# Optimization experiments

Measured on AMD Instinct MI355X. Metric: run time of the kernel, lower is better.

Reference implementation:

```python
import jax, jax.numpy as jnp
import numpy as np


def _layernorm(x, g, b, eps=1e-5):
    mu = jnp.mean(x, axis=-1, keepdims=True)
    var = jnp.mean(jnp.square(x - mu), axis=-1, keepdims=True)
    return (x - mu) * jax.lax.rsqrt(var + eps) * g + b


def setup_inputs() -> dict:
    key = jax.random.key(0)
    ks = jax.random.split(key, 8)
    dim, ctx_dim, heads, dim_head = 256, 256, 8, 64
    inner = heads * dim_head
    s = 0.02
    return {
        "x": jax.random.normal(ks[0], (4, dim, 64, 64), jnp.float32),
        "y": jax.random.normal(ks[1], (4, 1024, ctx_dim), jnp.float32),
        "ln_x_g": jnp.ones((dim,), jnp.float32),
        "ln_x_b": jnp.zeros((dim,), jnp.float32),
        "ln_y_g": jnp.ones((ctx_dim,), jnp.float32),
        "ln_y_b": jnp.zeros((ctx_dim,), jnp.float32),
        "Wq": jax.random.normal(ks[2], (dim, inner), jnp.float32) * s,
        "Wk": jax.random.normal(ks[3], (ctx_dim, inner), jnp.float32) * s,
        "Wv": jax.random.normal(ks[4], (ctx_dim, inner), jnp.float32) * s,
        "bv": jnp.zeros((inner,), jnp.float32),
        "Wo": jax.random.normal(ks[5], (inner, dim), jnp.float32) * s,
        "bo": jnp.zeros((dim,), jnp.float32),
    }


def reference(x, y, ln_x_g, ln_x_b, ln_y_g, ln_y_b, Wq, Wk, Wv, bv, Wo, bo):
    heads, dim_head = 8, 64
    b, c = x.shape[:2]
    # channel_last=False path: [b, c, H, W] -> [b, n, c]
    xn = x.reshape(b, c, -1).swapaxes(1, 2)
    xn = _layernorm(xn, ln_x_g, ln_x_b)          # note: x is reassigned in torch code
    yn = _layernorm(y, ln_y_g, ln_y_b)
    q = xn @ Wq                                   # [b, n, h*d]
    k = yn @ Wk                                   # [b, m, h*d]
    v = yn @ Wv + bv                              # [b, m, h*d]

    def split_heads(t):
        B, N, _ = t.shape
        return t.reshape(B, N, heads, dim_head).transpose(0, 2, 1, 3)  # [b, h, n, d]

    q, k, v = split_heads(q), split_heads(k), split_heads(v)
    attn = jnp.einsum("bhid,bhjd->bhij", q, k) * (dim_head ** -0.5)
    attn = jax.nn.softmax(attn, axis=-1)
    out = jnp.einsum("bhij,bhjd->bhid", attn, v)  # [b, h, n, d]
    out = out.transpose(0, 2, 1, 3).reshape(b, -1, heads * dim_head)
    out = out @ Wo + bo
    return xn + out  # residual with layernormed x (faithful to source)
```

## Files before the change

### kernel.cpp

```cpp
#include <hip/hip_runtime.h>
#include <hip/hip_bf16.h>
#include <cstddef>

#define BATCH 4
#define CDIM 256
#define HW 4096
#define MCTX 1024
#define CTX 256
#define HEADS 8
#define DHEAD 64
#define INNER 512

typedef __attribute__((ext_vector_type(8))) short bf16x8;
typedef __attribute__((ext_vector_type(4))) float f32x4;

static __device__ __forceinline__ ushort f2bf(float f) {
  __hip_bfloat16 h = __float2bfloat16(f);
  return *reinterpret_cast<ushort*>(&h);
}

__global__ __launch_bounds__(256) void ln_x_kernel(
    const float* __restrict__ x, const float* __restrict__ g,
    const float* __restrict__ bta, float* __restrict__ xn,
    ushort* __restrict__ xnbf) {
  const int blk = blockIdx.x;
  const int bi = blk / (HW / 32);
  const int n0 = (blk % (HW / 32)) * 32;
  __shared__ float xt[32][257];
  __shared__ float smu[32], srs[32];
  const int t = threadIdx.x;
  const int nl = t & 31;
  const int c0 = t >> 5;
  const float* xb = x + (size_t)bi * CDIM * HW;
  #pragma unroll
  for (int c = c0; c < CDIM; c += 8)
    xt[nl][c] = xb[(size_t)c * HW + n0 + nl];
  __syncthreads();
  const int col = t >> 3, j = t & 7;
  float s = 0.f, ss = 0.f;
  #pragma unroll
  for (int c = j; c < CDIM; c += 8) {
    float v = xt[col][c];
    s += v; ss += v * v;
  }
  #pragma unroll
  for (int off = 1; off < 8; off <<= 1) {
    s += __shfl_xor(s, off);
    ss += __shfl_xor(ss, off);
  }
  if (j == 0) {
    float mu = s * (1.f / CDIM);
    smu[col] = mu;
    srs[col] = rsqrtf(ss * (1.f / CDIM) - mu * mu + 1e-5f);
  }
  __syncthreads();
  const float gv = g[t], bvv = bta[t];
  float* xnb = xn + ((size_t)bi * HW + n0) * CDIM;
  ushort* xbb = xnbf + ((size_t)bi * HW + n0) * CDIM;
  #pragma unroll 4
  for (int n = 0; n < 32; ++n) {
    float val = (xt[n][t] - smu[n]) * srs[n] * gv + bvv;
    xnb[(size_t)n * CDIM + t] = val;
    xbb[(size_t)n * CDIM + t] = f2bf(val);
  }
}

__global__ __launch_bounds__(256) void ln_y_kernel(
    const float* __restrict__ y, const float* __restrict__ g,
    const float* __restrict__ bta, ushort* __restrict__ ynbf) {
  const int row = blockIdx.x * 4 + (threadIdx.x >> 6);
  const int t = threadIdx.x & 63;
  float4 v = ((const float4*)(y + (size_t)row * CTX))[t];
  float s = v.x + v.y + v.z + v.w;
  float ss = v.x * v.x + v.y * v.y + v.z * v.z + v.w * v.w;
  #pragma unroll
  for (int off = 1; off < 64; off <<= 1) {
    s += __shfl_xor(s, off);
    ss += __shfl_xor(ss, off);
  }
  float mu = s * (1.f / CTX);
  float rs = rsqrtf(ss * (1.f / CTX) - mu * mu + 1e-5f);
  float4 gv = ((const float4*)g)[t];
  float4 b4 = ((const float4*)bta)[t];
  ushort4 ob;
  ob.x = f2bf((v.x - mu) * rs * gv.x + b4.x);
  ob.y = f2bf((v.y - mu) * rs * gv.y + b4.y);
  ob.z = f2bf((v.z - mu) * rs * gv.z + b4.z);
  ob.w = f2bf((v.w - mu) * rs * gv.w + b4.w);
  *(ushort4*)(ynbf + (size_t)row * CTX + t * 4) = ob;
}

static __device__ __forceinline__ void wprep_body(
    const float* __restrict__ W, ushort* __restrict__ Wt, int K, int N) {
  __shared__ ushort T[64][65];
  const int k0 = blockIdx.y * 64, n0 = blockIdx.x * 64;
  const int t = threadIdx.x;
  #pragma unroll
  for (int rr = 0; rr < 4; ++rr) {
    int row = rr * 16 + (t >> 4);
    int c = (t & 15) * 4;
    float4 wv = *(const float4*)(W + (size_t)(k0 + row) * N + n0 + c);
    T[row][c + 0] = f2bf(wv.x); T[row][c + 1] = f2bf(wv.y);
    T[row][c + 2] = f2bf(wv.z); T[row][c + 3] = f2bf(wv.w);
  }
  __syncthreads();
  #pragma unroll
  for (int rr = 0; rr < 4; ++rr) {
    int nrow = rr * 16 + (t >> 4);
    int kc = (t & 15) * 4;
    ushort4 o;
    o.x = T[kc + 0][nrow]; o.y = T[kc + 1][nrow];
    o.z = T[kc + 2][nrow]; o.w = T[kc + 3][nrow];
    *(ushort4*)(Wt + (size_t)(n0 + nrow) * K + k0 + kc) = o;
  }
}

__global__ __launch_bounds__(256) void wprep3_kernel(
    const float* __restrict__ W0, const float* __restrict__ W1,
    const float* __restrict__ W2, ushort* __restrict__ T0,
    ushort* __restrict__ T1, ushort* __restrict__ T2) {
  const int z = blockIdx.z;
  const float* W = (z == 0) ? W0 : (z == 1) ? W1 : W2;
  ushort* Wt = (z == 0) ? T0 : (z == 1) ? T1 : T2;
  wprep_body(W, Wt, 256, 512);
}

__global__ __launch_bounds__(256) void wprep_kernel(
    const float* __restrict__ W, ushort* __restrict__ Wt, int K, int N) {
  wprep_body(W, Wt, K, N);
}

__global__ __launch_bounds__(256) void vtr_kernel(
    const ushort* __restrict__ v, ushort* __restrict__ vt) {
  const int bh = blockIdx.z, bi = bh >> 3, h = bh & 7;
  const int m0 = blockIdx.x * 64;
  __shared__ ushort T[64][65];
  const int t = threadIdx.x;
  #pragma unroll
  for (int rr = 0; rr < 4; ++rr) {
    int row = rr * 16 + (t >> 4);
    int c = (t & 15) * 4;
    ushort4 vv = *(const ushort4*)(v + (size_t)(bi * MCTX + m0 + row) * INNER + h * DHEAD + c);
    T[row][c + 0] = vv.x; T[row][c + 1] = vv.y;
    T[row][c + 2] = vv.z; T[row][c + 3] = vv.w;
  }
  __syncthreads();
  #pragma unroll
  for (int rr = 0; rr < 4; ++rr) {
    int drow = rr * 16 + (t >> 4);
    int mc = (t & 15) * 4;
    ushort4 o;
    o.x = T[mc + 0][drow]; o.y = T[mc + 1][drow];
    o.z = T[mc + 2][drow]; o.w = T[mc + 3][drow];
    *(ushort4*)(vt + (size_t)(bh * 64 + drow) * MCTX + m0 + mc) = o;
  }
}

template <bool HAS_BIAS, bool F32_RES_OUT>
__global__ __launch_bounds__(256) void mfma_gemm(
    const ushort* __restrict__ A, const ushort* __restrict__ Bt,
    const float* __restrict__ bias, const float* __restrict__ res,
    void* __restrict__ Cout, int M, int N, int K, float scale) {
  __shared__ ushort As[128 * 40];
  __shared__ ushort Bs[128 * 40];
  const int t = threadIdx.x;
  const int l = t & 63, w = t >> 6;
  const int lq = l & 15, lg = l >> 4;
  const int wr = w >> 1, wc = w & 1;
  const int m0 = blockIdx.y * 128, n0 = blockIdx.x * 128;
  f32x4 acc[4][4];
  #pragma unroll
  for (int mt = 0; mt < 4; ++mt)
    #pragma unroll
    for (int nt = 0; nt < 4; ++nt)
      #pragma unroll
      for (int e = 0; e < 4; ++e) acc[mt][nt][e] = 0.f;
  const int r = t >> 2, ch = (t & 3) * 8;
  for (int k0 = 0; k0 < K; k0 += 32) {
    uint4 a0 = *(const uint4*)(A + (size_t)(m0 + r) * K + k0 + ch);
    uint4 a1 = *(const uint4*)(A + (size_t)(m0 + r + 64) * K + k0 + ch);
    uint4 b0 = *(const uint4*)(Bt + (size_t)(n0 + r) * K + k0 + ch);
    uint4 b1 = *(const uint4*)(Bt + (size_t)(n0 + r + 64) * K + k0 + ch);
    __syncthreads();
    *(uint4*)(&As[r * 40 + ch]) = a0;
    *(uint4*)(&As[(r + 64) * 40 + ch]) = a1;
    *(uint4*)(&Bs[r * 40 + ch]) = b0;
    *(uint4*)(&Bs[(r + 64) * 40 + ch]) = b1;
    __syncthreads();
    bf16x8 af[4], bfr[4];
    #pragma unroll
    for (int mt = 0; mt < 4; ++mt)
      af[mt] = *(const bf16x8*)(&As[(wr * 64 + mt * 16 + lq) * 40 + lg * 8]);
    #pragma unroll
    for (int nt = 0; nt < 4; ++nt)
      bfr[nt] = *(const bf16x8*)(&Bs[(wc * 64 + nt * 16 + lq) * 40 + lg * 8]);
    #pragma unroll
    for (int mt = 0; mt < 4; ++mt)
      #pragma unroll
      for (int nt = 0; nt < 4; ++nt)
        acc[mt][nt] = __builtin_amdgcn_mfma_f32_16x16x32_bf16(
            af[mt], bfr[nt], acc[mt][nt], 0, 0, 0);
  }
  #pragma unroll
  for (int nt = 0; nt < 4; ++nt) {
    const int colc = n0 + wc * 64 + nt * 16 + lq;
    const float bcol = HAS_BIAS ? bias[colc] : 0.f;
    #pragma unroll
    for (int mt = 0; mt < 4; ++mt) {
      #pragma unroll
      for (int i = 0; i < 4; ++i) {
        const size_t row = (size_t)(m0 + wr * 64 + mt * 16 + lg * 4 + i);
        float v = acc[mt][nt][i] * scale + bcol;
        if (F32_RES_OUT) {
          ((float*)Cout)[row * N + colc] = v + res[row * N + colc];
        } else {
          ((ushort*)Cout)[row * N + colc] = f2bf(v);
        }
      }
    }
  }
}

__global__ __launch_bounds__(512, 4) void attn_mfma(
    const ushort* __restrict__ q, const ushort* __restrict__ k,
    const ushort* __restrict__ vt, ushort* __restrict__ ao) {
  const int bid = blockIdx.x + 16 * (blockIdx.y + 8 * blockIdx.z);
  const int swz = (bid & 7) * 64 + (bid >> 3);
  const int bi = swz >> 7;
  const int h = (swz >> 4) & 7;
  const int n0 = (swz & 15) * 256;
  __shared__ ushort Ks[2][64 * 64];
  __shared__ ushort Vs[2][64 * 64];
  __shared__ ushort Ps[8][2][16 * 64];
  const int t = threadIdx.x;
  const int l = t & 63, w = t >> 6;
  const int lq = l & 15, lg = l >> 4;

  bf16x8 bq[2][2];
  #pragma unroll
  for (int g = 0; g < 2; ++g) {
    const size_t qrow = (size_t)(bi * HW + n0 + w * 32 + g * 16 + lq);
    #pragma unroll
    for (int ks = 0; ks < 2; ++ks)
      bq[g][ks] = *(const bf16x8*)(q + qrow * INNER + h * DHEAD + ks * 32 + lg * 8);
  }

  float m_run[2] = {-1e30f, -1e30f}, l_run[2] = {0.f, 0.f};
  f32x4 oacc[2][4];
  #pragma unroll
  for (int g = 0; g < 2; ++g)
    #pragma unroll
    for (int dt = 0; dt < 4; ++dt)
      #pragma unroll
      for (int e = 0; e < 4; ++e) oacc[g][dt][e] = 0.f;

  const int rr = t >> 3, cc = (t & 7) * 8;
  const ushort* kptr = k + (size_t)(bi * MCTX + rr) * INNER + h * DHEAD + cc;
  const ushort* vptr = vt + (size_t)((bi * HEADS + h) * 64 + rr) * MCTX + cc;
  const int sidx = (rr * 64 + cc) ^ ((rr & 7) << 3);

  {
    uint4 k0v = *(const uint4*)(kptr);
    uint4 v0v = *(const uint4*)(vptr);
    *(uint4*)(&Ks[0][sidx]) = k0v;
    *(uint4*)(&Vs[0][sidx]) = v0v;
  }
  __syncthreads();

  auto softmax_group = [&](f32x4 (&scg)[4], float& mr, float& lr,
                           f32x4 (&oa)[4], ushort* psw) {
    float mloc = -1e30f;
    #pragma unroll
    for (int j = 0; j < 4; ++j)
      #pragma unroll
      for (int e = 0; e < 4; ++e) mloc = fmaxf(mloc, scg[j][e]);
    mloc = fmaxf(mloc, __shfl_xor(mloc, 16));
    mloc = fmaxf(mloc, __shfl_xor(mloc, 32));
    if (!__all((int)(mloc - mr <= 8.f))) {
      const float mnew = fmaxf(mr, mloc);
      const float corr = __builtin_amdgcn_exp2f(mr - mnew);
      lr *= corr;
      mr = mnew;
      #pragma unroll
      for (int i = 0; i < 4; ++i) {
        float ci = __shfl(corr, lg * 4 + i);
        #pragma unroll
        for (int dt = 0; dt < 4; ++dt) oa[dt][i] *= ci;
      }
    }
    float psum = 0.f;
    #pragma unroll
    for (int j = 0; j < 4; ++j)
      #pragma unroll
      for (int e = 0; e < 4; ++e) {
        float p = __builtin_amdgcn_exp2f(scg[j][e] - mr);
        scg[j][e] = p; psum += p;
      }
    psum += __shfl_xor(psum, 16);
    psum += __shfl_xor(psum, 32);
    lr += psum;
    #pragma unroll
    for (int j = 0; j < 4; ++j) {
      uint2 pk;
      pk.x = (uint)f2bf(scg[j][0]) | ((uint)f2bf(scg[j][1]) << 16);
      pk.y = (uint)f2bf(scg[j][2]) | ((uint)f2bf(scg[j][3]) << 16);
      *(uint2*)(psw + ((lq * 64 + j * 16 + lg * 4) ^ ((lq & 7) << 3))) = pk;
    }
  };

  #pragma unroll 2
  for (int m0 = 0; m0 < MCTX; m0 += 64) {
    const int buf = (m0 >> 6) & 1;
    const bool more = (m0 + 64) < MCTX;
    uint4 kpre{}, vpre{};
    if (more) {
      kpre = *(const uint4*)(kptr + (size_t)(m0 + 64) * INNER);
      vpre = *(const uint4*)(vptr + (m0 + 64));
    }
    f32x4 sc[2][4];
    #pragma unroll
    for (int g = 0; g < 2; ++g)
      #pragma unroll
      for (int j = 0; j < 4; ++j)
        #pragma unroll
        for (int e = 0; e < 4; ++e) sc[g][j][e] = 0.f;
    __builtin_amdgcn_s_setprio(1);
    #pragma unroll
    for (int j = 0; j < 4; ++j) {
      #pragma unroll
      for (int ks = 0; ks < 2; ++ks) {
        const int krow = j * 16 + lq;
        bf16x8 ak = *(const bf16x8*)(
            &Ks[buf][(krow * 64 + ks * 32 + lg * 8) ^ ((krow & 7) << 3)]);
        sc[0][j] = __builtin_amdgcn_mfma_f32_16x16x32_bf16(ak, bq[0][ks], sc[0][j], 0, 0, 0);
        sc[1][j] = __builtin_amdgcn_mfma_f32_16x16x32_bf16(ak, bq[1][ks], sc[1][j], 0, 0, 0);
      }
    }
    __builtin_amdgcn_s_setprio(0);
    softmax_group(sc[0], m_run[0], l_run[0], oacc[0], &Ps[w][0][0]);
    if (more) {
      *(uint4*)(&Ks[buf ^ 1][sidx]) = kpre;
      *(uint4*)(&Vs[buf ^ 1][sidx]) = vpre;
    }
    softmax_group(sc[1], m_run[1], l_run[1], oacc[1], &Ps[w][1][0]);
    bf16x8 pa[2][2];
    #pragma unroll
    for (int g = 0; g < 2; ++g)
      #pragma unroll
      for (int ks = 0; ks < 2; ++ks)
        pa[g][ks] = *(const bf16x8*)(
            &Ps[w][g][(lq * 64 + ks * 32 + lg * 8) ^ ((lq & 7) << 3)]);
    __builtin_amdgcn_s_setprio(1);
    #pragma unroll
    for (int dt = 0; dt < 4; ++dt) {
      #pragma unroll
      for (int ks = 0; ks < 2; ++ks) {
        const int vrow = dt * 16 + lq;
        bf16x8 vb = *(const bf16x8*)(
            &Vs[buf][(vrow * 64 + ks * 32 + lg * 8) ^ ((vrow & 7) << 3)]);
        oacc[0][dt] = __builtin_amdgcn_mfma_f32_16x16x32_bf16(pa[0][ks], vb, oacc[0][dt], 0, 0, 0);
        oacc[1][dt] = __builtin_amdgcn_mfma_f32_16x16x32_bf16(pa[1][ks], vb, oacc[1][dt], 0, 0, 0);
      }
    }
    __builtin_amdgcn_s_setprio(0);
    __syncthreads();
  }
  #pragma unroll
  for (int g = 0; g < 2; ++g) {
    const float rl = 1.f / l_run[g];
    #pragma unroll
    for (int i = 0; i < 4; ++i) {
      float li = __shfl(rl, lg * 4 + i);
      const size_t row = (size_t)(bi * HW + n0 + w * 32 + g * 16 + lg * 4 + i);
      #pragma unroll
      for (int dt = 0; dt < 4; ++dt)
        ao[row * INNER + h * DHEAD + dt * 16 + lq] = f2bf(oacc[g][dt][i] * li);
    }
  }
}

extern "C" void kernel_launch(void* const* d_in, const int* in_sizes, int n_in,
                              void* d_out, int out_size, void* d_ws, size_t ws_size,
                              hipStream_t stream) {
  const float* x     = (const float*)d_in[0];
  const float* y     = (const float*)d_in[1];
  const float* ln_xg = (const float*)d_in[2];
  const float* ln_xb = (const float*)d_in[3];
  const float* ln_yg = (const float*)d_in[4];
  const float* ln_yb = (const float*)d_in[5];
  const float* Wq    = (const float*)d_in[6];
  const float* Wk    = (const float*)d_in[7];
  const float* Wv    = (const float*)d_in[8];
  const float* bv    = (const float*)d_in[9];
  const float* Wo    = (const float*)d_in[10];
  const float* bo    = (const float*)d_in[11];
  float* out = (float*)d_out;

  char* p = (char*)d_ws;
  float*  xn   = (float*)p;  p += (size_t)16384 * 256 * 4;
  ushort* xnbf = (ushort*)p; p += (size_t)16384 * 256 * 2;
  ushort* ynbf = (ushort*)p; p += (size_t)4096 * 256 * 2;
  ushort* wtq  = (ushort*)p; p += (size_t)512 * 256 * 2;
  ushort* wtk  = (ushort*)p; p += (size_t)512 * 256 * 2;
  ushort* wtv  = (ushort*)p; p += (size_t)512 * 256 * 2;
  ushort* wto  = (ushort*)p; p += (size_t)256 * 512 * 2;
  ushort* qbf  = (ushort*)p; p += (size_t)16384 * 512 * 2;
  ushort* kbf  = (ushort*)p; p += (size_t)4096 * 512 * 2;
  ushort* vbf  = (ushort*)p; p += (size_t)4096 * 512 * 2;
  ushort* vtb  = (ushort*)p; p += (size_t)4096 * 512 * 2;
  ushort* aobf = (ushort*)p; p += (size_t)16384 * 512 * 2;

  wprep3_kernel<<<dim3(8, 4, 3), 256, 0, stream>>>(Wq, Wk, Wv, wtq, wtk, wtv);
  wprep_kernel<<<dim3(4, 8), 256, 0, stream>>>(Wo, wto, 512, 256);
  ln_x_kernel<<<dim3(BATCH * (HW / 32)), 256, 0, stream>>>(x, ln_xg, ln_xb, xn, xnbf);
  ln_y_kernel<<<dim3(BATCH * MCTX / 4), 256, 0, stream>>>(y, ln_yg, ln_yb, ynbf);
  mfma_gemm<false, false><<<dim3(4, 128), 256, 0, stream>>>(
      xnbf, wtq, nullptr, nullptr, qbf, 16384, 512, 256, 0.1803368801111204f);
  mfma_gemm<false, false><<<dim3(4, 32), 256, 0, stream>>>(
      ynbf, wtk, nullptr, nullptr, kbf, 4096, 512, 256, 1.f);
  mfma_gemm<true, false><<<dim3(4, 32), 256, 0, stream>>>(
      ynbf, wtv, bv, nullptr, vbf, 4096, 512, 256, 1.f);
  vtr_kernel<<<dim3(16, 1, 32), 256, 0, stream>>>(vbf, vtb);
  attn_mfma<<<dim3(HW / 256, HEADS, BATCH), 512, 0, stream>>>(qbf, kbf, vtb, aobf);
  mfma_gemm<true, true><<<dim3(2, 128), 256, 0, stream>>>(
      aobf, wto, bo, xn, out, 16384, 256, 512, 1.f);
}
```

Baseline: 124.7 us.

## Use direct global-to-LDS loads in attention, shrink blocks, merge K/V GEMMs

```diff
diff --git a/kernel.cpp b/kernel.cpp
--- a/kernel.cpp
+++ b/kernel.cpp
@@ -1,6 +1,7 @@
 #include <hip/hip_runtime.h>
 #include <hip/hip_bf16.h>
 #include <cstddef>
+#include <cstdint>
 
 #define BATCH 4
 #define CDIM 256
@@ -17,6 +18,13 @@
 static __device__ __forceinline__ ushort f2bf(float f) {
   __hip_bfloat16 h = __float2bfloat16(f);
   return *reinterpret_cast<ushort*>(&h);
+}
+
+static __device__ __forceinline__ void gload16(const void* g, void* l) {
+  __builtin_amdgcn_global_load_lds(
+      (const __attribute__((address_space(1))) void*)(uintptr_t)g,
+      (__attribute__((address_space(3))) void*)(uint32_t)(uintptr_t)l,
+      16, 0, 0);
 }
 
 __global__ __launch_bounds__(256) void ln_x_kernel(
@@ -156,18 +164,18 @@
   }
 }
 
-template <bool HAS_BIAS, bool F32_RES_OUT>
-__global__ __launch_bounds__(256) void mfma_gemm(
+template <bool F32_RES_OUT>
+static __device__ __forceinline__ void gemm_body(
     const ushort* __restrict__ A, const ushort* __restrict__ Bt,
     const float* __restrict__ bias, const float* __restrict__ res,
-    void* __restrict__ Cout, int M, int N, int K, float scale) {
+    void* __restrict__ Cout, int M, int N, int K, float scale,
+    int m0, int n0) {
   __shared__ ushort As[128 * 40];
   __shared__ ushort Bs[128 * 40];
   const int t = threadIdx.x;
   const int l = t & 63, w = t >> 6;
   const int lq = l & 15, lg = l >> 4;
   const int wr = w >> 1, wc = w & 1;
-  const int m0 = blockIdx.y * 128, n0 = blockIdx.x * 128;
   f32x4 acc[4][4];
   #pragma unroll
   for (int mt = 0; mt < 4; ++mt)
@@ -204,7 +212,7 @@
   #pragma unroll
   for (int nt = 0; nt < 4; ++nt) {
     const int colc = n0 + wc * 64 + nt * 16 + lq;
-    const float bcol = HAS_BIAS ? bias[colc] : 0.f;
+    const float bcol = bias ? bias[colc] : 0.f;
     #pragma unroll
     for (int mt = 0; mt < 4; ++mt) {
       #pragma unroll
@@ -221,17 +229,36 @@
   }
 }
 
-__global__ __launch_bounds__(512, 4) void attn_mfma(
+template <bool F32_RES_OUT>
+__global__ __launch_bounds__(256) void mfma_gemm(
+    const ushort* __restrict__ A, const ushort* __restrict__ Bt,
+    const float* __restrict__ bias, const float* __restrict__ res,
+    void* __restrict__ Cout, int M, int N, int K, float scale) {
+  gemm_body<F32_RES_OUT>(A, Bt, bias, res, Cout, M, N, K, scale,
+                         blockIdx.y * 128, blockIdx.x * 128);
+}
+
+__global__ __launch_bounds__(256) void mfma_gemm_kv(
+    const ushort* __restrict__ A, const ushort* __restrict__ BtK,
+    const ushort* __restrict__ BtV, const float* __restrict__ bv,
+    ushort* __restrict__ Ck, ushort* __restrict__ Cv) {
+  const bool isV = blockIdx.x >= 4;
+  gemm_body<false>(A, isV ? BtV : BtK, isV ? bv : nullptr, nullptr,
+                   isV ? (void*)Cv : (void*)Ck, 4096, 512, 256, 1.f,
+                   blockIdx.y * 128, (blockIdx.x & 3) * 128);
+}
+
+__global__ __launch_bounds__(256, 4) void attn_mfma(
     const ushort* __restrict__ q, const ushort* __restrict__ k,
     const ushort* __restrict__ vt, ushort* __restrict__ ao) {
-  const int bid = blockIdx.x + 16 * (blockIdx.y + 8 * blockIdx.z);
-  const int swz = (bid & 7) * 64 + (bid >> 3);
-  const int bi = swz >> 7;
-  const int h = (swz >> 4) & 7;
-  const int n0 = (swz & 15) * 256;
+  const int bid = blockIdx.x + 32 * (blockIdx.y + 8 * blockIdx.z);
+  const int swz = (bid & 7) * 128 + (bid >> 3);
+  const int bi = swz >> 8;
+  const int h = (swz >> 5) & 7;
+  const int n0 = (swz & 31) * 128;
   __shared__ ushort Ks[2][64 * 64];
   __shared__ ushort Vs[2][64 * 64];
-  __shared__ ushort Ps[8][2][16 * 64];
+  __shared__ ushort Ps[4][16 * 64];
   const int t = threadIdx.x;
   const int l = t & 63, w = t >> 6;
   const int lq = l & 15, lg = l >> 4;
@@ -254,26 +281,31 @@
       #pragma unroll
       for (int e = 0; e < 4; ++e) oacc[g][dt][e] = 0.f;
 
-  const int rr = t >> 3, cc = (t & 7) * 8;
-  const ushort* kptr = k + (size_t)(bi * MCTX + rr) * INNER + h * DHEAD + cc;
-  const ushort* vptr = vt + (size_t)((bi * HEADS + h) * 64 + rr) * MCTX + cc;
-  const int sidx = (rr * 64 + cc) ^ ((rr & 7) << 3);
+  const int rrA = w * 16 + (l >> 3);
+  const int rrB = rrA + 8;
+  const int cA = ((l & 7) ^ (rrA & 7)) * 8;
+  const int cB = ((l & 7) ^ (rrB & 7)) * 8;
+  const ushort* kA = k + (size_t)(bi * MCTX + rrA) * INNER + h * DHEAD + cA;
+  const ushort* kB = k + (size_t)(bi * MCTX + rrB) * INNER + h * DHEAD + cB;
+  const ushort* vA = vt + (size_t)((bi * HEADS + h) * 64 + rrA) * MCTX + cA;
+  const ushort* vB = vt + (size_t)((bi * HEADS + h) * 64 + rrB) * MCTX + cB;
+  const int lb0 = w * 1024, lb1 = w * 1024 + 512;
 
   {
-    uint4 k0v = *(const uint4*)(kptr);
-    uint4 v0v = *(const uint4*)(vptr);
-    *(uint4*)(&Ks[0][sidx]) = k0v;
-    *(uint4*)(&Vs[0][sidx]) = v0v;
+    gload16(kA, &Ks[0][lb0]);
+    gload16(kB, &Ks[0][lb1]);
+    gload16(vA, &Vs[0][lb0]);
+    gload16(vB, &Vs[0][lb1]);
   }
   __syncthreads();
 
-  auto softmax_group = [&](f32x4 (&scg)[4], float& mr, float& lr,
-                           f32x4 (&oa)[4], ushort* psw) {
-    float mloc = -1e30f;
-    #pragma unroll
-    for (int j = 0; j < 4; ++j)
-      #pragma unroll
-      for (int e = 0; e < 4; ++e) mloc = fmaxf(mloc, scg[j][e]);
+  auto sm_compute = [&](f32x4 (&scg)[4], float& mr, float& lr,
+                        f32x4 (&oa)[4], uint2 (&pk)[4]) {
+    f32x4 mv;
+    #pragma unroll
+    for (int e = 0; e < 4; ++e)
+      mv[e] = fmaxf(fmaxf(scg[0][e], scg[1][e]), fmaxf(scg[2][e], scg[3][e]));
+    float mloc = fmaxf(fmaxf(mv[0], mv[1]), fmaxf(mv[2], mv[3]));
     mloc = fmaxf(mloc, __shfl_xor(mloc, 16));
     mloc = fmaxf(mloc, __shfl_xor(mloc, 32));
     if (!__all((int)(mloc - mr <= 8.f))) {
@@ -288,34 +320,35 @@
         for (int dt = 0; dt < 4; ++dt) oa[dt][i] *= ci;
       }
     }
-    float psum = 0.f;
     #pragma unroll
     for (int j = 0; j < 4; ++j)
       #pragma unroll
-      for (int e = 0; e < 4; ++e) {
-        float p = __builtin_amdgcn_exp2f(scg[j][e] - mr);
-        scg[j][e] = p; psum += p;
-      }
+      for (int e = 0; e < 4; ++e)
+        scg[j][e] = __builtin_amdgcn_exp2f(scg[j][e] - mr);
+    f32x4 s4;
+    #pragma unroll
+    for (int e = 0; e < 4; ++e)
+      s4[e] = (scg[0][e] + scg[1][e]) + (scg[2][e] + scg[3][e]);
+    float psum = (s4[0] + s4[1]) + (s4[2] + s4[3]);
     psum += __shfl_xor(psum, 16);
     psum += __shfl_xor(psum, 32);
     lr += psum;
     #pragma unroll
     for (int j = 0; j < 4; ++j) {
-      uint2 pk;
-      pk.x = (uint)f2bf(scg[j][0]) | ((uint)f2bf(scg[j][1]) << 16);
-      pk.y = (uint)f2bf(scg[j][2]) | ((uint)f2bf(scg[j][3]) << 16);
-      *(uint2*)(psw + ((lq * 64 + j * 16 + lg * 4) ^ ((lq & 7) << 3))) = pk;
+      pk[j].x = (uint)f2bf(scg[j][0]) | ((uint)f2bf(scg[j][1]) << 16);
+      pk[j].y = (uint)f2bf(scg[j][2]) | ((uint)f2bf(scg[j][3]) << 16);
     }
   };
 
-  #pragma unroll 2
   for (int m0 = 0; m0 < MCTX; m0 += 64) {
     const int buf = (m0 >> 6) & 1;
     const bool more = (m0 + 64) < MCTX;
-    uint4 kpre{}, vpre{};
     if (more) {
-      kpre = *(const uint4*)(kptr + (size_t)(m0 + 64) * INNER);
-      vpre = *(const uint4*)(vptr + (m0 + 64));
+      const int mn = m0 + 64;
+      gload16(kA + (size_t)mn * INNER, &Ks[buf ^ 1][lb0]);
+      gload16(kB + (size_t)mn * INNER, &Ks[buf ^ 1][lb1]);
+      gload16(vA + mn, &Vs[buf ^ 1][lb0]);
+      gload16(vB + mn, &Vs[buf ^ 1][lb1]);
     }
     f32x4 sc[2][4];
     #pragma unroll
@@ -337,19 +370,24 @@
       }
     }
     __builtin_amdgcn_s_setprio(0);
-    softmax_group(sc[0], m_run[0], l_run[0], oacc[0], &Ps[w][0][0]);
-    if (more) {
-      *(uint4*)(&Ks[buf ^ 1][sidx]) = kpre;
-      *(uint4*)(&Vs[buf ^ 1][sidx]) = vpre;
-    }
-    softmax_group(sc[1], m_run[1], l_run[1], oacc[1], &Ps[w][1][0]);
-    bf16x8 pa[2][2];
-    #pragma unroll
-    for (int g = 0; g < 2; ++g)
-      #pragma unroll
-      for (int ks = 0; ks < 2; ++ks)
-        pa[g][ks] = *(const bf16x8*)(
-            &Ps[w][g][(lq * 64 + ks * 32 + lg * 8) ^ ((lq & 7) << 3)]);
+    uint2 pk0[4], pk1[4];
+    sm_compute(sc[0], m_run[0], l_run[0], oacc[0], pk0);
+    #pragma unroll
+    for (int j = 0; j < 4; ++j)
+      *(uint2*)(&Ps[w][(lq * 64 + j * 16 + lg * 4) ^ ((lq & 7) << 3)]) = pk0[j];
+    sm_compute(sc[1], m_run[1], l_run[1], oacc[1], pk1);
+    bf16x8 pa0[2], pa1[2];
+    #pragma unroll
+    for (int ks = 0; ks < 2; ++ks)
+      pa0[ks] = *(const bf16x8*)(
+          &Ps[w][(lq * 64 + ks * 32 + lg * 8) ^ ((lq & 7) << 3)]);
+    #pragma unroll
+    for (int j = 0; j < 4; ++j)
+      *(uint2*)(&Ps[w][(lq * 64 + j * 16 + lg * 4) ^ ((lq & 7) << 3)]) = pk1[j];
+    #pragma unroll
+    for (int ks = 0; ks < 2; ++ks)
+      pa1[ks] = *(const bf16x8*)(
+          &Ps[w][(lq * 64 + ks * 32 + lg * 8) ^ ((lq & 7) << 3)]);
     __builtin_amdgcn_s_setprio(1);
     #pragma unroll
     for (int dt = 0; dt < 4; ++dt) {
@@ -358,8 +396,8 @@
         const int vrow = dt * 16 + lq;
         bf16x8 vb = *(const bf16x8*)(
             &Vs[buf][(vrow * 64 + ks * 32 + lg * 8) ^ ((vrow & 7) << 3)]);
-        oacc[0][dt] = __builtin_amdgcn_mfma_f32_16x16x32_bf16(pa[0][ks], vb, oacc[0][dt], 0, 0, 0);
-        oacc[1][dt] = __builtin_amdgcn_mfma_f32_16x16x32_bf16(pa[1][ks], vb, oacc[1][dt], 0, 0, 0);
+        oacc[0][dt] = __builtin_amdgcn_mfma_f32_16x16x32_bf16(pa0[ks], vb, oacc[0][dt], 0, 0, 0);
+        oacc[1][dt] = __builtin_amdgcn_mfma_f32_16x16x32_bf16(pa1[ks], vb, oacc[1][dt], 0, 0, 0);
       }
     }
     __builtin_amdgcn_s_setprio(0);
@@ -414,14 +452,11 @@
   wprep_kernel<<<dim3(4, 8), 256, 0, stream>>>(Wo, wto, 512, 256);
   ln_x_kernel<<<dim3(BATCH * (HW / 32)), 256, 0, stream>>>(x, ln_xg, ln_xb, xn, xnbf);
   ln_y_kernel<<<dim3(BATCH * MCTX / 4), 256, 0, stream>>>(y, ln_yg, ln_yb, ynbf);
-  mfma_gemm<false, false><<<dim3(4, 128), 256, 0, stream>>>(
+  mfma_gemm<false><<<dim3(4, 128), 256, 0, stream>>>(
       xnbf, wtq, nullptr, nullptr, qbf, 16384, 512, 256, 0.1803368801111204f);
-  mfma_gemm<false, false><<<dim3(4, 32), 256, 0, stream>>>(
-      ynbf, wtk, nullptr, nullptr, kbf, 4096, 512, 256, 1.f);
-  mfma_gemm<true, false><<<dim3(4, 32), 256, 0, stream>>>(
-      ynbf, wtv, bv, nullptr, vbf, 4096, 512, 256, 1.f);
+  mfma_gemm_kv<<<dim3(8, 32), 256, 0, stream>>>(ynbf, wtk, wtv, bv, kbf, vbf);
   vtr_kernel<<<dim3(16, 1, 32), 256, 0, stream>>>(vbf, vtb);
-  attn_mfma<<<dim3(HW / 256, HEADS, BATCH), 512, 0, stream>>>(qbf, kbf, vtb, aobf);
-  mfma_gemm<true, true><<<dim3(2, 128), 256, 0, stream>>>(
+  attn_mfma<<<dim3(HW / 128, HEADS, BATCH), 256, 0, stream>>>(qbf, kbf, vtb, aobf);
+  mfma_gemm<true><<<dim3(2, 128), 256, 0, stream>>>(
       aobf, wto, bo, xn, out, 16384, 256, 512, 1.f);
 }
```

New measurement: 129.1 us. 3.5% more time.

## Use direct global-to-LDS loads in GEMM, merge K/V projections, tree-reduce softmax

Applied to the files above, without the earlier changes.

```diff
diff --git a/kernel.cpp b/kernel.cpp
--- a/kernel.cpp
+++ b/kernel.cpp
@@ -1,6 +1,7 @@
 #include <hip/hip_runtime.h>
 #include <hip/hip_bf16.h>
 #include <cstddef>
+#include <cstdint>
 
 #define BATCH 4
 #define CDIM 256
@@ -17,6 +18,13 @@
 static __device__ __forceinline__ ushort f2bf(float f) {
   __hip_bfloat16 h = __float2bfloat16(f);
   return *reinterpret_cast<ushort*>(&h);
+}
+
+static __device__ __forceinline__ void gload16(const void* g, void* l) {
+  __builtin_amdgcn_global_load_lds(
+      (const __attribute__((address_space(1))) void*)(uintptr_t)g,
+      (__attribute__((address_space(3))) void*)(uint32_t)(uintptr_t)l,
+      16, 0, 0);
 }
 
 __global__ __launch_bounds__(256) void ln_x_kernel(
@@ -156,18 +164,18 @@
   }
 }
 
-template <bool HAS_BIAS, bool F32_RES_OUT>
-__global__ __launch_bounds__(256) void mfma_gemm(
+template <bool F32_RES_OUT>
+static __device__ __forceinline__ void gemm_body(
     const ushort* __restrict__ A, const ushort* __restrict__ Bt,
     const float* __restrict__ bias, const float* __restrict__ res,
-    void* __restrict__ Cout, int M, int N, int K, float scale) {
-  __shared__ ushort As[128 * 40];
-  __shared__ ushort Bs[128 * 40];
+    void* __restrict__ Cout, int M, int N, int K, float scale,
+    int m0, int n0) {
+  __shared__ ushort As[128 * 64];
+  __shared__ ushort Bs[128 * 64];
   const int t = threadIdx.x;
   const int l = t & 63, w = t >> 6;
   const int lq = l & 15, lg = l >> 4;
   const int wr = w >> 1, wc = w & 1;
-  const int m0 = blockIdx.y * 128, n0 = blockIdx.x * 128;
   f32x4 acc[4][4];
   #pragma unroll
   for (int mt = 0; mt < 4; ++mt)
@@ -175,36 +183,46 @@
     for (int nt = 0; nt < 4; ++nt)
       #pragma unroll
       for (int e = 0; e < 4; ++e) acc[mt][nt][e] = 0.f;
-  const int r = t >> 2, ch = (t & 3) * 8;
-  for (int k0 = 0; k0 < K; k0 += 32) {
-    uint4 a0 = *(const uint4*)(A + (size_t)(m0 + r) * K + k0 + ch);
-    uint4 a1 = *(const uint4*)(A + (size_t)(m0 + r + 64) * K + k0 + ch);
-    uint4 b0 = *(const uint4*)(Bt + (size_t)(n0 + r) * K + k0 + ch);
-    uint4 b1 = *(const uint4*)(Bt + (size_t)(n0 + r + 64) * K + k0 + ch);
+  const int srow = w * 8 + (l >> 3);
+  const int scol = ((l & 7) ^ (l >> 3)) * 8;
+  const ushort* pA = A + (size_t)(m0 + srow) * K + scol;
+  const ushort* pB = Bt + (size_t)(n0 + srow) * K + scol;
+  const int dbase = w * 512;
+  for (int k0 = 0; k0 < K; k0 += 64) {
+    if (k0) __syncthreads();
+    #pragma unroll
+    for (int i = 0; i < 4; ++i) {
+      gload16(pA + (size_t)(i * 32) * K + k0, &As[i * 2048 + dbase]);
+      gload16(pB + (size_t)(i * 32) * K + k0, &Bs[i * 2048 + dbase]);
+    }
     __syncthreads();
-    *(uint4*)(&As[r * 40 + ch]) = a0;
-    *(uint4*)(&As[(r + 64) * 40 + ch]) = a1;
-    *(uint4*)(&Bs[r * 40 + ch]) = b0;
-    *(uint4*)(&Bs[(r + 64) * 40 + ch]) = b1;
-    __syncthreads();
-    bf16x8 af[4], bfr[4];
-    #pragma unroll
-    for (int mt = 0; mt < 4; ++mt)
-      af[mt] = *(const bf16x8*)(&As[(wr * 64 + mt * 16 + lq) * 40 + lg * 8]);
-    #pragma unroll
-    for (int nt = 0; nt < 4; ++nt)
-      bfr[nt] = *(const bf16x8*)(&Bs[(wc * 64 + nt * 16 + lq) * 40 + lg * 8]);
-    #pragma unroll
-    for (int mt = 0; mt < 4; ++mt)
-      #pragma unroll
-      for (int nt = 0; nt < 4; ++nt)
-        acc[mt][nt] = __builtin_amdgcn_mfma_f32_16x16x32_bf16(
-            af[mt], bfr[nt], acc[mt][nt], 0, 0, 0);
+    #pragma unroll
+    for (int ks = 0; ks < 2; ++ks) {
+      bf16x8 af[4], bfr[4];
+      #pragma unroll
+      for (int mt = 0; mt < 4; ++mt) {
+        const int R = wr * 64 + mt * 16 + lq;
+        af[mt] = *(const bf16x8*)(
+            &As[R * 64 + ((ks * 32 + lg * 8) ^ ((R & 7) * 8))]);
+      }
+      #pragma unroll
+      for (int nt = 0; nt < 4; ++nt) {
+        const int R = wc * 64 + nt * 16 + lq;
+        bfr[nt] = *(const bf16x8*)(
+            &Bs[R * 64 + ((ks * 32 + lg * 8) ^ ((R & 7) * 8))]);
+      }
+      #pragma unroll
+      for (int mt = 0; mt < 4; ++mt)
+        #pragma unroll
+        for (int nt = 0; nt < 4; ++nt)
+          acc[mt][nt] = __builtin_amdgcn_mfma_f32_16x16x32_bf16(
+              af[mt], bfr[nt], acc[mt][nt], 0, 0, 0);
+    }
   }
   #pragma unroll
   for (int nt = 0; nt < 4; ++nt) {
     const int colc = n0 + wc * 64 + nt * 16 + lq;
-    const float bcol = HAS_BIAS ? bias[colc] : 0.f;
+    const float bcol = bias ? bias[colc] : 0.f;
     #pragma unroll
     for (int mt = 0; mt < 4; ++mt) {
       #pragma unroll
@@ -219,6 +237,25 @@
       }
     }
   }
+}
+
+template <bool F32_RES_OUT>
+__global__ __launch_bounds__(256) void mfma_gemm(
+    const ushort* __restrict__ A, const ushort* __restrict__ Bt,
+    const float* __restrict__ bias, const float* __restrict__ res,
+    void* __restrict__ Cout, int M, int N, int K, float scale) {
+  gemm_body<F32_RES_OUT>(A, Bt, bias, res, Cout, M, N, K, scale,
+                         blockIdx.y * 128, blockIdx.x * 128);
+}
+
+__global__ __launch_bounds__(256) void mfma_gemm_kv(
+    const ushort* __restrict__ A, const ushort* __restrict__ BtK,
+    const ushort* __restrict__ BtV, const float* __restrict__ bv,
+    ushort* __restrict__ Ck, ushort* __restrict__ Cv) {
+  const bool isV = blockIdx.x >= 4;
+  gemm_body<false>(A, isV ? BtV : BtK, isV ? bv : nullptr, nullptr,
+                   isV ? (void*)Cv : (void*)Ck, 4096, 512, 256, 1.f,
+                   blockIdx.y * 128, (blockIdx.x & 3) * 128);
 }
 
 __global__ __launch_bounds__(512, 4) void attn_mfma(
@@ -269,11 +306,11 @@
 
   auto softmax_group = [&](f32x4 (&scg)[4], float& mr, float& lr,
                            f32x4 (&oa)[4], ushort* psw) {
-    float mloc = -1e30f;
-    #pragma unroll
-    for (int j = 0; j < 4; ++j)
-      #pragma unroll
-      for (int e = 0; e < 4; ++e) mloc = fmaxf(mloc, scg[j][e]);
+    f32x4 mv;
+    #pragma unroll
+    for (int e = 0; e < 4; ++e)
+      mv[e] = fmaxf(fmaxf(scg[0][e], scg[1][e]), fmaxf(scg[2][e], scg[3][e]));
+    float mloc = fmaxf(fmaxf(mv[0], mv[1]), fmaxf(mv[2], mv[3]));
     mloc = fmaxf(mloc, __shfl_xor(mloc, 16));
     mloc = fmaxf(mloc, __shfl_xor(mloc, 32));
     if (!__all((int)(mloc - mr <= 8.f))) {
@@ -288,14 +325,16 @@
         for (int dt = 0; dt < 4; ++dt) oa[dt][i] *= ci;
       }
     }
-    float psum = 0.f;
     #pragma unroll
     for (int j = 0; j < 4; ++j)
       #pragma unroll
-      for (int e = 0; e < 4; ++e) {
-        float p = __builtin_amdgcn_exp2f(scg[j][e] - mr);
-        scg[j][e] = p; psum += p;
-      }
+      for (int e = 0; e < 4; ++e)
+        scg[j][e] = __builtin_amdgcn_exp2f(scg[j][e] - mr);
+    f32x4 s4;
+    #pragma unroll
+    for (int e = 0; e < 4; ++e)
+      s4[e] = (scg[0][e] + scg[1][e]) + (scg[2][e] + scg[3][e]);
+    float psum = (s4[0] + s4[1]) + (s4[2] + s4[3]);
     psum += __shfl_xor(psum, 16);
     psum += __shfl_xor(psum, 32);
     lr += psum;
@@ -414,14 +453,11 @@
   wprep_kernel<<<dim3(4, 8), 256, 0, stream>>>(Wo, wto, 512, 256);
   ln_x_kernel<<<dim3(BATCH * (HW / 32)), 256, 0, stream>>>(x, ln_xg, ln_xb, xn, xnbf);
   ln_y_kernel<<<dim3(BATCH * MCTX / 4), 256, 0, stream>>>(y, ln_yg, ln_yb, ynbf);
-  mfma_gemm<false, false><<<dim3(4, 128), 256, 0, stream>>>(
+  mfma_gemm<false><<<dim3(4, 128), 256, 0, stream>>>(
       xnbf, wtq, nullptr, nullptr, qbf, 16384, 512, 256, 0.1803368801111204f);
-  mfma_gemm<false, false><<<dim3(4, 32), 256, 0, stream>>>(
-      ynbf, wtk, nullptr, nullptr, kbf, 4096, 512, 256, 1.f);
-  mfma_gemm<true, false><<<dim3(4, 32), 256, 0, stream>>>(
-      ynbf, wtv, bv, nullptr, vbf, 4096, 512, 256, 1.f);
+  mfma_gemm_kv<<<dim3(8, 32), 256, 0, stream>>>(ynbf, wtk, wtv, bv, kbf, vbf);
   vtr_kernel<<<dim3(16, 1, 32), 256, 0, stream>>>(vbf, vtb);
   attn_mfma<<<dim3(HW / 256, HEADS, BATCH), 512, 0, stream>>>(qbf, kbf, vtb, aobf);
-  mfma_gemm<true, true><<<dim3(2, 128), 256, 0, stream>>>(
+  mfma_gemm<true><<<dim3(2, 128), 256, 0, stream>>>(
       aobf, wto, bo, xn, out, 16384, 256, 512, 1.f);
 }
```

Measured after the change: 119.1 us. 1.05x faster.
